# Optimization experiments

Measured on AMD Instinct MI355X. Metric: run time of the kernel, lower is better.

## Reference

```python
import jax, jax.numpy as jnp
import numpy as np

B, L, H = 4, 2048, 1024
NQ, NKV, D = 8, 2, 256
I, V = 3584, 16384
EPS = 1e-6
THETA = 1e7
ROPE_DIM = 64

def rmsnorm(x, w, eps=EPS):
    xf = x.astype(jnp.float32)
    rms = jax.lax.rsqrt(jnp.mean(xf * xf, axis=-1, keepdims=True) + eps)
    return (xf * rms).astype(x.dtype) * w

def apply_rope(x, positions):
    # x: [B, H, L, D]; rotate first ROPE_DIM dims, interleaved pairs
    n_pairs = ROPE_DIM // 2
    inv_freq = THETA ** (-2.0 * jnp.arange(n_pairs, dtype=jnp.float32) / ROPE_DIM)
    freqs = positions.astype(jnp.float32)[:, None] * inv_freq[None, :]  # [L, n_pairs]
    cos = jnp.cos(freqs)[None, None, :, :]
    sin = jnp.sin(freqs)[None, None, :, :]
    b, h, l, d = x.shape
    xr = x[..., :ROPE_DIM].reshape(b, h, l, n_pairs, 2)
    x0, x1 = xr[..., 0], xr[..., 1]
    r0 = x0 * cos - x1 * sin
    r1 = x0 * sin + x1 * cos
    rotated = jnp.stack([r0, r1], axis=-1).reshape(b, h, l, ROPE_DIM)
    return jnp.concatenate([rotated, x[..., ROPE_DIM:]], axis=-1)

def setup_inputs() -> dict:
    key = jax.random.key(0)
    ks = jax.random.split(key, 12)
    s = 0.02
    return {
        "embeddings": jax.random.normal(ks[0], (B, L, H), jnp.float32),
        "hidden_states": jax.random.normal(ks[1], (B, L, H), jnp.float32),
        "pre_emb_w": jnp.ones((H,), jnp.float32),
        "pre_hid_w": jnp.ones((H,), jnp.float32),
        "fc_w": jax.random.normal(ks[2], (H, 2 * H), jnp.float32) * s,
        "in_ln_w": jnp.ones((H,), jnp.float32),
        "q_w": jax.random.normal(ks[3], (2 * NQ * D, H), jnp.float32) * s,
        "k_w": jax.random.normal(ks[4], (NKV * D, H), jnp.float32) * s,
        "v_w": jax.random.normal(ks[5], (NKV * D, H), jnp.float32) * s,
        "o_w": jax.random.normal(ks[6], (H, NQ * D), jnp.float32) * s,
        "qn_w": jnp.ones((D,), jnp.float32),
        "kn_w": jnp.ones((D,), jnp.float32),
        "post_ln_w": jnp.ones((H,), jnp.float32),
        "gate_w": jax.random.normal(ks[7], (I, H), jnp.float32) * s,
        "up_w": jax.random.normal(ks[8], (I, H), jnp.float32) * s,
        "down_w": jax.random.normal(ks[9], (H, I), jnp.float32) * s,
        "norm_w": jnp.ones((H,), jnp.float32),
        "lm_w": jax.random.normal(ks[10], (V, H), jnp.float32) * s,
    }

def _attention(x, q_w, k_w, v_w, o_w, qn_w, kn_w):
    b, l, _ = x.shape
    qg = (x @ q_w.T).reshape(b, l, NQ, 2, D)
    q = qg[:, :, :, 0, :]
    gate = qg[:, :, :, 1, :]
    k = (x @ k_w.T).reshape(b, l, NKV, D)
    v = (x @ v_w.T).reshape(b, l, NKV, D)
    q = rmsnorm(q, qn_w)
    k = rmsnorm(k, kn_w)
    groups = NQ // NKV
    k = jnp.repeat(k, groups, axis=2)  # [B, L, NQ, D]
    v = jnp.repeat(v, groups, axis=2)
    q, k, v = (t.transpose(0, 2, 1, 3) for t in (q, k, v))  # [B, NQ, L, D]
    positions = jnp.arange(l)
    q = apply_rope(q, positions)
    k = apply_rope(k, positions)
    scores = jnp.einsum('bhqd,bhkd->bhqk', q, k) / jnp.sqrt(jnp.float32(D))
    causal = jnp.tril(jnp.ones((l, l), jnp.bool_))
    scores = jnp.where(causal[None, None], scores, jnp.finfo(scores.dtype).min)
    attn = jax.nn.softmax(scores, axis=-1)
    out = jnp.einsum('bhqk,bhkd->bhqd', attn, v)
    out = out.transpose(0, 2, 1, 3).reshape(b, l, NQ * D)
    out = out * jax.nn.sigmoid(gate.reshape(b, l, NQ * D))
    return out @ o_w.T

def reference(embeddings, hidden_states, pre_emb_w, pre_hid_w, fc_w, in_ln_w,
              q_w, k_w, v_w, o_w, qn_w, kn_w, post_ln_w, gate_w, up_w, down_w,
              norm_w, lm_w):
    x = jnp.concatenate([rmsnorm(embeddings, pre_emb_w),
                         rmsnorm(hidden_states, pre_hid_w)], axis=-1)
    x = x @ fc_w.T
    residual = x
    x = rmsnorm(x, in_ln_w)
    x = _attention(x, q_w, k_w, v_w, o_w, qn_w, kn_w)
    x = residual + x
    residual = x
    x = rmsnorm(x, post_ln_w)
    x = (jax.nn.silu(x @ gate_w.T) * (x @ up_w.T)) @ down_w.T
    x = residual + x
    x = rmsnorm(x, norm_w)
    return x @ lm_w.T
```

## Files before the change

### kernel.cpp

```cpp
#include <hip/hip_runtime.h>

typedef __bf16 bf16;
typedef __bf16 bf16x8 __attribute__((ext_vector_type(8)));
typedef __bf16 bf16x4 __attribute__((ext_vector_type(4)));
typedef float f32x4 __attribute__((ext_vector_type(4)));

__device__ inline f32x4 mfma16(bf16x8 a, bf16x8 b, f32x4 c) {
    return __builtin_amdgcn_mfma_f32_16x16x32_bf16(a, b, c, 0, 0, 0);
}

__device__ __forceinline__ void async_cp16(const void* g, void* l) {
    __builtin_amdgcn_global_load_lds(
        (__attribute__((address_space(1))) char*)g,
        (__attribute__((address_space(3))) char*)l,
        16, 0, 0);
}

__global__ __launch_bounds__(256) void w2b_kernel(const float* __restrict__ s,
                                                  bf16* __restrict__ d)
{
    const size_t i = ((size_t)blockIdx.x * 256 + threadIdx.x) * 4;
    const float4 f = *(const float4*)(s + i);
    bf16x4 t;
    t[0] = (bf16)f.x; t[1] = (bf16)f.y; t[2] = (bf16)f.z; t[3] = (bf16)f.w;
    *(bf16x4*)(d + i) = t;
}

__global__ __launch_bounds__(256) void w2b_qkv_kernel(
    const float* __restrict__ qw, const float* __restrict__ kw,
    const float* __restrict__ vw, bf16* __restrict__ dq)
{
    int bid = blockIdx.x;
    const float* s; bf16* d;
    if (bid < 4096)      { s = qw; d = dq; }
    else if (bid < 4608) { s = kw; d = dq + 4194304; bid -= 4096; }
    else                 { s = vw; d = dq + 4718592; bid -= 4608; }
    const size_t i = ((size_t)bid * 256 + threadIdx.x) * 4;
    const float4 f = *(const float4*)(s + i);
    bf16x4 t;
    t[0] = (bf16)f.x; t[1] = (bf16)f.y; t[2] = (bf16)f.z; t[3] = (bf16)f.w;
    *(bf16x4*)(d + i) = t;
}

__global__ __launch_bounds__(256) void w2b_gu_kernel(
    const float* __restrict__ gw, const float* __restrict__ uw, bf16* __restrict__ dg)
{
    int bid = blockIdx.x;
    const float* s; bf16* d;
    if (bid < 3584) { s = gw; d = dg; }
    else            { s = uw; d = dg + 3670016; bid -= 3584; }
    const size_t i = ((size_t)bid * 256 + threadIdx.x) * 4;
    const float4 f = *(const float4*)(s + i);
    bf16x4 t;
    t[0] = (bf16)f.x; t[1] = (bf16)f.y; t[2] = (bf16)f.z; t[3] = (bf16)f.w;
    *(bf16x4*)(d + i) = t;
}

template <int EPI>
__global__ __launch_bounds__(256) void gemm_kernel(
    const bf16* __restrict__ A, const bf16* __restrict__ B,
    const float* __restrict__ res, float* __restrict__ Cout,
    int M, int N, int K)
{
    __shared__ bf16 As[2][128][64];
    __shared__ bf16 Bs[2][128][64];
    const int tid = threadIdx.x;
    const int wave = tid >> 6, lane = tid & 63;
    const int quad = lane >> 4, l16 = lane & 15;
    const int xsw = l16 & 7;

    const int nby = M >> 7, nbx = N >> 7;
    const int nwg = nbx * nby;
    int bid = blockIdx.x;
    {
        const int q = nwg >> 3, r = nwg & 7;
        const int x = bid & 7, loc = bid >> 3;
        bid = (x < r ? x * (q + 1) : r * (q + 1) + (x - r) * q) + loc;
    }
    const int pg = nbx << 3;
    const int g = bid / pg, rem = bid - g * pg;
    const int by = (g << 3) + (rem & 7);
    const int bx = rem >> 3;
    const int row0 = by << 7, col0 = bx << 7;
    const int wrow = ((wave >> 1) << 6), wcol = ((wave & 1) << 6);

    f32x4 acc[4][4] = {};

    const int srow = tid >> 3;
    const int scol = ((tid & 7) ^ (srow & 7)) * 8;
    const bf16* Ag = A + (size_t)(row0 + srow) * K + scol;
    const bf16* Bg = B + (size_t)(col0 + srow) * K + scol;
    const size_t K32 = (size_t)32 * K;

#define STG128(BUF, KB) do { \
    _Pragma("unroll") for (int q = 0; q < 4; ++q) { \
        async_cp16(Ag + q * K32 + (KB), &As[BUF][0][0] + q * 2048 + wave * 512); \
        async_cp16(Bg + q * K32 + (KB), &Bs[BUF][0][0] + q * 2048 + wave * 512); } } while (0)

    const int NT = K >> 6;
    STG128(0, 0);
    __syncthreads();
    for (int t = 0; t < NT; ++t) {
        const int c = t & 1, n = c ^ 1;
        if (t + 1 < NT) STG128(n, (t + 1) * 64);
        bf16x8 af[8], bfr[8];
#pragma unroll
        for (int i = 0; i < 4; ++i) {
            af[i * 2 + 0] = *(const bf16x8*)(&As[c][wrow + i * 16 + l16][(quad ^ xsw) * 8]);
            af[i * 2 + 1] = *(const bf16x8*)(&As[c][wrow + i * 16 + l16][((4 + quad) ^ xsw) * 8]);
        }
#pragma unroll
        for (int j = 0; j < 4; ++j) {
            bfr[j * 2 + 0] = *(const bf16x8*)(&Bs[c][wcol + j * 16 + l16][(quad ^ xsw) * 8]);
            bfr[j * 2 + 1] = *(const bf16x8*)(&Bs[c][wcol + j * 16 + l16][((4 + quad) ^ xsw) * 8]);
        }
#pragma unroll
        for (int i = 0; i < 4; ++i)
#pragma unroll
            for (int j = 0; j < 4; ++j) {
                acc[i][j] = mfma16(af[i * 2 + 0], bfr[j * 2 + 0], acc[i][j]);
                acc[i][j] = mfma16(af[i * 2 + 1], bfr[j * 2 + 1], acc[i][j]);
            }
        __syncthreads();
    }
#undef STG128

#pragma unroll
    for (int i = 0; i < 4; ++i) {
        const int row = row0 + wrow + i * 16 + quad * 4;
#pragma unroll
        for (int j = 0; j < 4; ++j) {
            const int col = col0 + wcol + j * 16 + l16;
#pragma unroll
            for (int r = 0; r < 4; ++r) {
                const size_t idx = (size_t)(row + r) * N + col;
                float v = acc[i][j][r];
                if (EPI == 1) Cout[idx] = v + res[idx];
                else          Cout[idx] = v;
            }
        }
    }
}

template <int EPI>
__global__ __launch_bounds__(512, 2) void gemm256_kernel(
    const bf16* __restrict__ A, const bf16* __restrict__ B,
    const float* __restrict__ res, float* __restrict__ Cout,
    bf16* __restrict__ hout, int M, int N, int K)
{
    __shared__ bf16 As[2][2][128][64];
    __shared__ bf16 Bs[2][2][128][64];
    const int tid = threadIdx.x;
    const int wid = tid >> 6, lane = tid & 63;
    const int quad = lane >> 4, l16 = lane & 15;
    const int wm = wid >> 2, wn = wid & 3;
    const int xsw = l16 & 7;
    const int bofs = (wn & 1) * 64;

    const int nby = M >> 8, nbx = N >> 8;
    const int nwg = nbx * nby;
    int bid = blockIdx.x;
    {
        const int q = nwg >> 3, r = nwg & 7;
        const int x = bid & 7, loc = bid >> 3;
        bid = (x < r ? x * (q + 1) : r * (q + 1) + (x - r) * q) + loc;
    }
    const int pg = nbx << 3;
    const int g = bid / pg, rem = bid - g * pg;
    const int by = (g << 3) + (rem & 7);
    const int bx = rem >> 3;
    const int row0 = by << 8, col0 = bx << 8;

    const int srow = tid >> 3;
    const int scol = ((tid & 7) ^ ((tid >> 3) & 7)) * 8;
    const bf16* Abase = A + (size_t)(row0 + srow) * K + scol;
    const bf16* Bbase = B + (size_t)(col0 + srow) * K + scol;
    const size_t K64 = (size_t)K * 64;
    const size_t K128 = (size_t)K * 128;

    f32x4 acc[8][4] = {};
    bf16x8 af[8], bf0[4], bf1[4];

#define STG_A(BUF, HH, KB) do { \
    const bf16* _g = Abase + (size_t)(HH) * K128 + (KB); \
    bf16* _l = &As[BUF][HH][0][0] + wid * 512; \
    async_cp16(_g, _l); \
    async_cp16(_g + K64, _l + 4096); } while (0)
#define STG_B(BUF, HH, KB) do { \
    const bf16* _g = Bbase + (size_t)(HH) * K128 + (KB); \
    bf16* _l = &Bs[BUF][HH][0][0] + wid * 512; \
    async_cp16(_g, _l); \
    async_cp16(_g + K64, _l + 4096); } while (0)

#define RD_A(BUF, RH) do { \
    const bf16 (*Ah_)[64] = As[BUF][wm]; \
    _Pragma("unroll") for (int f = 0; f < 4; ++f) { \
        af[f*2+0] = *(const bf16x8*)(&Ah_[(RH)*64 + f*16 + l16][(quad ^ xsw) * 8]); \
        af[f*2+1] = *(const bf16x8*)(&Ah_[(RH)*64 + f*16 + l16][((4 + quad) ^ xsw) * 8]); } } while (0)

#define RD_B(BUF, CH, BF) do { \
    const bf16 (*Bh_)[64] = Bs[BUF][wn >> 1]; \
    _Pragma("unroll") for (int f = 0; f < 2; ++f) { \
        BF[f*2+0] = *(const bf16x8*)(&Bh_[bofs + (CH)*32 + f*16 + l16][(quad ^ xsw) * 8]); \
        BF[f*2+1] = *(const bf16x8*)(&Bh_[bofs + (CH)*32 + f*16 + l16][((4 + quad) ^ xsw) * 8]); } } while (0)

#define MFMA_Q(RH, CH, BF) do { \
    _Pragma("unroll") for (int f = 0; f < 4; ++f) \
    _Pragma("unroll") for (int f2 = 0; f2 < 2; ++f2) { \
        acc[(RH)*4+f][(CH)*2+f2] = mfma16(af[f*2+0], BF[f2*2+0], acc[(RH)*4+f][(CH)*2+f2]); \
        acc[(RH)*4+f][(CH)*2+f2] = mfma16(af[f*2+1], BF[f2*2+1], acc[(RH)*4+f][(CH)*2+f2]); } } while (0)

    const int NT = K >> 6;
    STG_A(0, 0, 0); STG_A(0, 1, 0); STG_B(0, 0, 0); STG_B(0, 1, 0);
    if (NT > 1) {
        STG_A(1, 0, 64); STG_A(1, 1, 64); STG_B(1, 0, 64); STG_B(1, 1, 64);
        asm volatile("s_waitcnt vmcnt(8)" ::: "memory");
    } else {
        asm volatile("s_waitcnt vmcnt(0)" ::: "memory");
    }
    __builtin_amdgcn_sched_barrier(0);
    __builtin_amdgcn_s_barrier();
    RD_A(0, 0); RD_B(0, 0, bf0); RD_B(0, 1, bf1);
    __builtin_amdgcn_sched_barrier(0);

    for (int t = 0; t < NT; ++t) {
        const int c = t & 1, n = c ^ 1;
        const int kb1 = (t + 1) << 6, kb2 = (t + 2) << 6;
        if (t >= 1 && t + 1 < NT) { STG_A(n, 0, kb1); STG_A(n, 1, kb1); }
        asm volatile("s_waitcnt lgkmcnt(4)" ::: "memory");
        __builtin_amdgcn_sched_barrier(0);
        __builtin_amdgcn_s_setprio(1);
        MFMA_Q(0, 0, bf0);
        __builtin_amdgcn_s_setprio(0);
        asm volatile("s_waitcnt lgkmcnt(0)" ::: "memory");
        __builtin_amdgcn_sched_barrier(0);
        __builtin_amdgcn_s_setprio(1);
        MFMA_Q(0, 1, bf1);
        __builtin_amdgcn_s_setprio(0);
        RD_A(c, 1);
        __builtin_amdgcn_sched_barrier(0);
        __builtin_amdgcn_s_barrier();
        if (t + 2 < NT) { STG_B(c, 0, kb2); STG_B(c, 1, kb2); }
        asm volatile("s_waitcnt lgkmcnt(0)" ::: "memory");
        __builtin_amdgcn_sched_barrier(0);
        __builtin_amdgcn_s_setprio(1);
        MFMA_Q(1, 0, bf0);
        MFMA_Q(1, 1, bf1);
        __builtin_amdgcn_s_setprio(0);
        if (t + 1 < NT) {
            if (t + 2 < NT) { asm volatile("s_waitcnt vmcnt(4)" ::: "memory"); }
            else            { asm volatile("s_waitcnt vmcnt(0)" ::: "memory"); }
            __builtin_amdgcn_sched_barrier(0);
            RD_A(n, 0); RD_B(n, 0, bf0); RD_B(n, 1, bf1);
            __builtin_amdgcn_sched_barrier(0);
        }
        __builtin_amdgcn_s_barrier();
    }
#undef STG_A
#undef STG_B
#undef RD_A
#undef RD_B
#undef MFMA_Q

#pragma unroll
    for (int fr = 0; fr < 8; ++fr) {
        const int row = row0 + wm * 128 + fr * 16 + quad * 4;
#pragma unroll
        for (int fc = 0; fc < 4; ++fc) {
            const int col = col0 + wn * 64 + fc * 16 + l16;
#pragma unroll
            for (int r = 0; r < 4; ++r) {
                const size_t idx = (size_t)(row + r) * N + col;
                float v = acc[fr][fc][r];
                if (EPI == 1) {
                    Cout[idx] = v + res[idx];
                } else if (EPI == 2) {
                    const float gg = res[idx];
                    hout[idx] = (bf16)(gg * (1.f / (1.f + __expf(-gg))) * v);
                } else {
                    Cout[idx] = v;
                }
            }
        }
    }
}

__global__ __launch_bounds__(256) void prenorm_kernel(
    const float* __restrict__ emb, const float* __restrict__ hid,
    const float* __restrict__ we, const float* __restrict__ wh,
    bf16* __restrict__ xcat)
{
    const int rr = blockIdx.x * 4 + (threadIdx.x >> 6);
    const int lane = threadIdx.x & 63;
    const int half = rr & 1, row = rr >> 1;
    const float* x = (half ? hid : emb) + (size_t)row * 1024;
    const float* w = half ? wh : we;
    float4 v[4]; float ss = 0.f;
#pragma unroll
    for (int j = 0; j < 4; ++j) {
        v[j] = *(const float4*)(x + (size_t)(lane + 64 * j) * 4);
        ss += v[j].x * v[j].x + v[j].y * v[j].y + v[j].z * v[j].z + v[j].w * v[j].w;
    }
#pragma unroll
    for (int m = 32; m; m >>= 1) ss += __shfl_xor(ss, m, 64);
    const float rms = rsqrtf(ss * (1.f / 1024.f) + 1e-6f);
    bf16* o = xcat + (size_t)row * 2048 + half * 1024;
#pragma unroll
    for (int j = 0; j < 4; ++j) {
        const int d = (lane + 64 * j) * 4;
        float4 wv = *(const float4*)(w + d);
        bf16x4 t;
        t[0] = (bf16)(v[j].x * rms * wv.x);
        t[1] = (bf16)(v[j].y * rms * wv.y);
        t[2] = (bf16)(v[j].z * rms * wv.z);
        t[3] = (bf16)(v[j].w * rms * wv.w);
        *(bf16x4*)(o + d) = t;
    }
}

__global__ __launch_bounds__(256) void rmsnorm_kernel(
    const float* __restrict__ xin, const float* __restrict__ w, bf16* __restrict__ out)
{
    const int row = blockIdx.x * 4 + (threadIdx.x >> 6);
    const int lane = threadIdx.x & 63;
    const float* x = xin + (size_t)row * 1024;
    float4 v[4]; float ss = 0.f;
#pragma unroll
    for (int j = 0; j < 4; ++j) {
        v[j] = *(const float4*)(x + (size_t)(lane + 64 * j) * 4);
        ss += v[j].x * v[j].x + v[j].y * v[j].y + v[j].z * v[j].z + v[j].w * v[j].w;
    }
#pragma unroll
    for (int m = 32; m; m >>= 1) ss += __shfl_xor(ss, m, 64);
    const float rms = rsqrtf(ss * (1.f / 1024.f) + 1e-6f);
    bf16* o = out + (size_t)row * 1024;
#pragma unroll
    for (int j = 0; j < 4; ++j) {
        const int d = (lane + 64 * j) * 4;
        float4 wv = *(const float4*)(w + d);
        bf16x4 t;
        t[0] = (bf16)(v[j].x * rms * wv.x);
        t[1] = (bf16)(v[j].y * rms * wv.y);
        t[2] = (bf16)(v[j].z * rms * wv.z);
        t[3] = (bf16)(v[j].w * rms * wv.w);
        *(bf16x4*)(o + d) = t;
    }
}

__global__ __launch_bounds__(256) void qprep_kernel(
    const float* __restrict__ qg, const float* __restrict__ qn_w, bf16* __restrict__ qa)
{
    const int row = blockIdx.x * 4 + (threadIdx.x >> 6);
    const int lane = threadIdx.x & 63;
    const int h = row & 7, bl = row >> 3;
    const int l = bl & 2047, b = bl >> 11;
    const float* x = qg + (size_t)row * 512;
    float4 v = *(const float4*)(x + lane * 4);
    float ss = v.x * v.x + v.y * v.y + v.z * v.z + v.w * v.w;
#pragma unroll
    for (int m = 32; m; m >>= 1) ss += __shfl_xor(ss, m, 64);
    const float rms = rsqrtf(ss * (1.f / 256.f) + 1e-6f);
    const float4 wv = *(const float4*)(qn_w + lane * 4);
    float y0 = v.x * rms * wv.x, y1 = v.y * rms * wv.y;
    float y2 = v.z * rms * wv.z, y3 = v.w * rms * wv.w;
    if (lane < 16) {
        const float inv0 = powf(1e7f, -(float)(4 * lane) * (1.f / 64.f));
        const float inv1 = powf(1e7f, -(float)(4 * lane + 2) * (1.f / 64.f));
        const float a0 = (float)l * inv0, a1 = (float)l * inv1;
        const float c0 = cosf(a0), s0 = sinf(a0), c1 = cosf(a1), s1 = sinf(a1);
        const float r0 = y0 * c0 - y1 * s0, r1 = y0 * s0 + y1 * c0;
        const float r2 = y2 * c1 - y3 * s1, r3 = y2 * s1 + y3 * c1;
        y0 = r0; y1 = r1; y2 = r2; y3 = r3;
    }
    bf16* o = qa + ((size_t)((b * 8 + h) * 2048 + l)) * 256 + lane * 4;
    bf16x4 t;
    t[0] = (bf16)(y0 * 0.0625f); t[1] = (bf16)(y1 * 0.0625f);
    t[2] = (bf16)(y2 * 0.0625f); t[3] = (bf16)(y3 * 0.0625f);
    *(bf16x4*)o = t;
}

__global__ __launch_bounds__(256) void kprep_kernel(
    const float* __restrict__ kvf, const float* __restrict__ kn_w, bf16* __restrict__ ka)
{
    const int row = blockIdx.x * 4 + (threadIdx.x >> 6);
    const int lane = threadIdx.x & 63;
    const int kv = row & 1, bl = row >> 1;
    const int l = bl & 2047, b = bl >> 11;
    const float* x = kvf + (size_t)bl * 1024 + kv * 256;
    float4 v = *(const float4*)(x + lane * 4);
    float ss = v.x * v.x + v.y * v.y + v.z * v.z + v.w * v.w;
#pragma unroll
    for (int m = 32; m; m >>= 1) ss += __shfl_xor(ss, m, 64);
    const float rms = rsqrtf(ss * (1.f / 256.f) + 1e-6f);
    const float4 wv = *(const float4*)(kn_w + lane * 4);
    float y0 = v.x * rms * wv.x, y1 = v.y * rms * wv.y;
    float y2 = v.z * rms * wv.z, y3 = v.w * rms * wv.w;
    if (lane < 16) {
        const float inv0 = powf(1e7f, -(float)(4 * lane) * (1.f / 64.f));
        const float inv1 = powf(1e7f, -(float)(4 * lane + 2) * (1.f / 64.f));
        const float a0 = (float)l * inv0, a1 = (float)l * inv1;
        const float c0 = cosf(a0), s0 = sinf(a0), c1 = cosf(a1), s1 = sinf(a1);
        const float r0 = y0 * c0 - y1 * s0, r1 = y0 * s0 + y1 * c0;
        const float r2 = y2 * c1 - y3 * s1, r3 = y2 * s1 + y3 * c1;
        y0 = r0; y1 = r1; y2 = r2; y3 = r3;
    }
    bf16* o = ka + ((size_t)((b * 2 + kv) * 2048 + l)) * 256 + lane * 4;
    bf16x4 t;
    t[0] = (bf16)y0; t[1] = (bf16)y1; t[2] = (bf16)y2; t[3] = (bf16)y3;
    *(bf16x4*)o = t;
}

__global__ __launch_bounds__(256) void vprep_kernel(const float* __restrict__ kvf,
                                                    bf16* __restrict__ vt)
{
    __shared__ float t[64][65];
    const int l0 = blockIdx.x << 6;
    const int d0 = blockIdx.y << 6;
    const int b = blockIdx.z >> 1, kv = blockIdx.z & 1;
    const int tx = threadIdx.x & 63, ty = threadIdx.x >> 6;
    const float* src = kvf + (size_t)b * 2048 * 1024 + 512 + kv * 256;
#pragma unroll
    for (int j = 0; j < 16; ++j) {
        const int l = ty + j * 4;
        t[l][tx] = src[(size_t)(l0 + l) * 1024 + d0 + tx];
    }
    __syncthreads();
    bf16* dst = vt + (size_t)(b * 2 + kv) * 256 * 2048;
#pragma unroll
    for (int j = 0; j < 16; ++j) {
        const int d = ty + j * 4;
        dst[(size_t)(d0 + d) * 2048 + l0 + tx] = (bf16)t[tx][d];
    }
}

__global__ __launch_bounds__(256) void attn_kernel(
    const bf16* __restrict__ qa, const bf16* __restrict__ ka,
    const bf16* __restrict__ vt, const float* __restrict__ qg,
    bf16* __restrict__ ag)
{
    __shared__ bf16 Ks[32 * 256];
    __shared__ bf16 Vt[256 * 32];
    __shared__ bf16 Pw[4 * 16 * 32];
    const int tid = threadIdx.x;
    const int wave = tid >> 6, lane = tid & 63;
    const int quad = lane >> 4, l16 = lane & 15;
    const int bid = blockIdx.x;
    const int j = bid & 15, h = (bid >> 4) & 7, b = bid >> 7;
    const int kvh = h >> 2;
    const bf16* qptr = qa + ((size_t)(b * 8 + h)) * 2048 * 256;
    const bf16* kptr = ka + ((size_t)(b * 2 + kvh)) * 2048 * 256;
    const bf16* vptr = vt + ((size_t)(b * 2 + kvh)) * 256 * 2048;

    for (int s = 0; s < 2; ++s) {
        const int qt = s ? (31 - j) : j;
        const int qbase = qt * 64 + wave * 16;

        bf16x8 qf[8];
#pragma unroll
        for (int db = 0; db < 8; ++db)
            qf[db] = *(const bf16x8*)(qptr + (size_t)(qbase + l16) * 256 + db * 32 + quad * 8);

        f32x4 o_acc[16] = {};
        float m_i[4], l_i[4];
#pragma unroll
        for (int r = 0; r < 4; ++r) { m_i[r] = -1e30f; l_i[r] = 0.f; }

        const int ntiles = qt * 2 + 2;
        for (int kt = 0; kt < ntiles; ++kt) {
            const int kvs = kt * 32;
#pragma unroll
            for (int c = 0; c < 4; ++c) {
                const int idx = tid + c * 256;
                const int kr = idx >> 5, kc32 = idx & 31;
                *(bf16x8*)(&Ks[kr * 256 + (kc32 ^ (kr & 7)) * 8]) =
                    *(const bf16x8*)(kptr + (size_t)(kvs + kr) * 256 + kc32 * 8);
                const int vd = idx >> 2, vc = (idx & 3) * 8;
                *(bf16x8*)(&Vt[vd * 32 + vc]) = *(const bf16x8*)(vptr + (size_t)vd * 2048 + kvs + vc);
            }
            __syncthreads();

            f32x4 s0 = {}, s1 = {};
#pragma unroll
            for (int db = 0; db < 8; ++db) {
                const int ch = (db * 4 + quad) ^ (l16 & 7);
                bf16x8 k0 = *(const bf16x8*)(&Ks[l16 * 256 + ch * 8]);
                bf16x8 k1 = *(const bf16x8*)(&Ks[(16 + l16) * 256 + ch * 8]);
                s0 = mfma16(qf[db], k0, s0);
                s1 = mfma16(qf[db], k1, s1);
            }

            float alpha[4], p0v[4], p1v[4];
#pragma unroll
            for (int r = 0; r < 4; ++r) {
                const int qrow = qbase + quad * 4 + r;
                float a0 = (kvs + l16 > qrow) ? -1e30f : s0[r];
                float a1 = (kvs + 16 + l16 > qrow) ? -1e30f : s1[r];
                float mx = fmaxf(a0, a1);
#pragma unroll
                for (int m = 8; m; m >>= 1) mx = fmaxf(mx, __shfl_xor(mx, m, 64));
                const float mnew = fmaxf(m_i[r], mx);
                const float a = __expf(m_i[r] - mnew);
                const float p0 = __expf(a0 - mnew);
                const float p1 = __expf(a1 - mnew);
                float ps = p0 + p1;
#pragma unroll
                for (int m = 8; m; m >>= 1) ps += __shfl_xor(ps, m, 64);
                l_i[r] = l_i[r] * a + ps;
                m_i[r] = mnew;
                alpha[r] = a; p0v[r] = p0; p1v[r] = p1;
            }
#pragma unroll
            for (int t = 0; t < 16; ++t) {
                f32x4 o = o_acc[t];
                o[0] *= alpha[0]; o[1] *= alpha[1]; o[2] *= alpha[2]; o[3] *= alpha[3];
                o_acc[t] = o;
            }
            bf16* pw = &Pw[wave * 16 * 32];
#pragma unroll
            for (int r = 0; r < 4; ++r) {
                pw[(quad * 4 + r) * 32 + l16]      = (bf16)p0v[r];
                pw[(quad * 4 + r) * 32 + 16 + l16] = (bf16)p1v[r];
            }
            __syncthreads();
            const bf16x8 pa = *(const bf16x8*)(&pw[l16 * 32 + quad * 8]);
#pragma unroll
            for (int t = 0; t < 16; ++t) {
                bf16x8 vfr = *(const bf16x8*)(&Vt[(t * 16 + l16) * 32 + quad * 8]);
                o_acc[t] = mfma16(pa, vfr, o_acc[t]);
            }
            __syncthreads();
        }

#pragma unroll
        for (int r = 0; r < 4; ++r) {
            const float inv = 1.f / l_i[r];
            const int row = qbase + quad * 4 + r;
            const float* gr = qg + ((size_t)((b * 2048 + row) * 8 + h)) * 512 + 256;
            bf16* ar = ag + ((size_t)(b * 2048 + row)) * 2048 + h * 256;
#pragma unroll
            for (int t = 0; t < 16; ++t) {
                const int d = t * 16 + l16;
                const float o = o_acc[t][r] * inv;
                const float gg = gr[d];
                ar[d] = (bf16)(o * (1.f / (1.f + __expf(-gg))));
            }
        }
    }
}

extern "C" void kernel_launch(void* const* d_in, const int* in_sizes, int n_in,
                              void* d_out, int out_size, void* d_ws, size_t ws_size,
                              hipStream_t stream)
{
    const float* emb       = (const float*)d_in[0];
    const float* hid       = (const float*)d_in[1];
    const float* pre_emb_w = (const float*)d_in[2];
    const float* pre_hid_w = (const float*)d_in[3];
    const float* fc_w      = (const float*)d_in[4];
    const float* in_ln_w   = (const float*)d_in[5];
    const float* q_w       = (const float*)d_in[6];
    const float* k_w       = (const float*)d_in[7];
    const float* v_w       = (const float*)d_in[8];
    const float* o_w       = (const float*)d_in[9];
    const float* qn_w      = (const float*)d_in[10];
    const float* kn_w      = (const float*)d_in[11];
    const float* post_ln_w = (const float*)d_in[12];
    const float* gate_w    = (const float*)d_in[13];
    const float* up_w      = (const float*)d_in[14];
    const float* down_w    = (const float*)d_in[15];
    const float* norm_w    = (const float*)d_in[16];
    const float* lm_w      = (const float*)d_in[17];
    float* out = (float*)d_out;
    char* ws = (char*)d_ws;

    float* xres = (float*)(ws + 0);
    bf16*  xln  = (bf16*)(ws + 33554432);
    char*  C    = ws + 50331648;
    char*  D    = ws + 184549376;
    char*  E    = ws + 318767104;
    float* qg   = (float*)C;
    float* gf   = (float*)C;
    bf16*  xcat = (bf16*)D;
    float* kvf  = (float*)(D + 33554432);
    bf16*  ag   = (bf16*)(D + 67108864);
    bf16*  qa   = (bf16*)E;
    bf16*  ka   = (bf16*)(E + 33554432);
    bf16*  va   = (bf16*)(E + 41943040);
    bf16*  hb   = (bf16*)E;
    bf16*  wbC  = (bf16*)C;
    bf16*  wbD  = (bf16*)D;
    bf16*  wkv  = (bf16*)D + 4194304;
    bf16*  wbDt = (bf16*)(D + 117440512);

    prenorm_kernel<<<4096, 256, 0, stream>>>(emb, hid, pre_emb_w, pre_hid_w, xcat);

    w2b_kernel<<<2048, 256, 0, stream>>>(fc_w, wbC);
    gemm_kernel<0><<<512, 256, 0, stream>>>(xcat, wbC, nullptr, xres, 8192, 1024, 2048);
    rmsnorm_kernel<<<2048, 256, 0, stream>>>(xres, in_ln_w, xln);

    w2b_qkv_kernel<<<5120, 256, 0, stream>>>(q_w, k_w, v_w, wbD);
    gemm256_kernel<0><<<512, 512, 0, stream>>>(xln, wbD, nullptr, qg, nullptr, 8192, 4096, 1024);
    gemm_kernel<0><<<512, 256, 0, stream>>>(xln, wkv, nullptr, kvf, 8192, 1024, 1024);

    qprep_kernel<<<16384, 256, 0, stream>>>(qg, qn_w, qa);
    kprep_kernel<<<4096, 256, 0, stream>>>(kvf, kn_w, ka);
    vprep_kernel<<<dim3(32, 4, 8), 256, 0, stream>>>(kvf, va);
    attn_kernel<<<512, 256, 0, stream>>>(qa, ka, va, qg, ag);

    w2b_kernel<<<2048, 256, 0, stream>>>(o_w, wbC);
    gemm_kernel<1><<<512, 256, 0, stream>>>(ag, wbC, xres, xres, 8192, 1024, 2048);
    rmsnorm_kernel<<<2048, 256, 0, stream>>>(xres, post_ln_w, xln);

    w2b_gu_kernel<<<7168, 256, 0, stream>>>(gate_w, up_w, wbDt);
    gemm256_kernel<0><<<448, 512, 0, stream>>>(xln, wbDt, nullptr, gf, nullptr, 8192, 3584, 1024);
    gemm256_kernel<2><<<448, 512, 0, stream>>>(xln, wbDt + 3670016, gf, nullptr, hb, 8192, 3584, 1024);

    w2b_kernel<<<3584, 256, 0, stream>>>(down_w, wbC);
    gemm_kernel<1><<<512, 256, 0, stream>>>(hb, wbC, xres, xres, 8192, 1024, 3584);
    rmsnorm_kernel<<<2048, 256, 0, stream>>>(xres, norm_w, xln);

    w2b_kernel<<<16384, 256, 0, stream>>>(lm_w, wbC);
    gemm256_kernel<0><<<2048, 512, 0, stream>>>(xln, wbC, nullptr, out, nullptr, 8192, 16384, 1024);
}
```

Before: 1.710 ms.

## Double-buffer K/V tiles in attention via async global-to-LDS loads

The attention kernel now keeps two LDS buffers for K and V tiles. It prefetches the next tile with global_load_lds while the current one is being computed, and swaps explicit waitcnt/barrier sequences in for the __syncthreads calls. The weight-conversion kernel becomes grid-stride with a fixed grid of 2048 blocks, which cuts block count for the large lm_head and down weights. The aim is to hide K/V load latency behind MFMA work. In exchange the kernel uses twice the LDS, which may lower occupancy, and the Pw write/read now relies on an intra-wave lgkmcnt wait rather than a block barrier.

```diff
diff --git a/kernel.cpp b/kernel.cpp
--- a/kernel.cpp
+++ b/kernel.cpp
@@ -17,13 +17,15 @@
 }
 
 __global__ __launch_bounds__(256) void w2b_kernel(const float* __restrict__ s,
-                                                  bf16* __restrict__ d)
-{
-    const size_t i = ((size_t)blockIdx.x * 256 + threadIdx.x) * 4;
-    const float4 f = *(const float4*)(s + i);
-    bf16x4 t;
-    t[0] = (bf16)f.x; t[1] = (bf16)f.y; t[2] = (bf16)f.z; t[3] = (bf16)f.w;
-    *(bf16x4*)(d + i) = t;
+                                                  bf16* __restrict__ d, int nvec4)
+{
+    for (size_t i = (size_t)blockIdx.x * 256 + threadIdx.x; i < (size_t)nvec4;
+         i += (size_t)2048 * 256) {
+        const float4 f = *(const float4*)(s + i * 4);
+        bf16x4 t;
+        t[0] = (bf16)f.x; t[1] = (bf16)f.y; t[2] = (bf16)f.z; t[3] = (bf16)f.w;
+        *(bf16x4*)(d + i * 4) = t;
+    }
 }
 
 __global__ __launch_bounds__(256) void w2b_qkv_kernel(
@@ -438,8 +440,8 @@
     const bf16* __restrict__ vt, const float* __restrict__ qg,
     bf16* __restrict__ ag)
 {
-    __shared__ bf16 Ks[32 * 256];
-    __shared__ bf16 Vt[256 * 32];
+    __shared__ bf16 Ks[2][32 * 256];
+    __shared__ bf16 Vt[2][256 * 32];
     __shared__ bf16 Pw[4 * 16 * 32];
     const int tid = threadIdx.x;
     const int wave = tid >> 6, lane = tid & 63;
@@ -451,6 +453,17 @@
     const bf16* kptr = ka + ((size_t)(b * 2 + kvh)) * 2048 * 256;
     const bf16* vptr = vt + ((size_t)(b * 2 + kvh)) * 256 * 2048;
 
+#define STAGE_KV(BUF, KVS) do { \
+    _Pragma("unroll") for (int c = 0; c < 4; ++c) { \
+        const int idx = c * 256 + tid; \
+        const int kr = idx >> 5; \
+        const int kcs = ((idx & 31) ^ (kr & 7)) * 8; \
+        async_cp16(kptr + (size_t)((KVS) + kr) * 256 + kcs, \
+                   &Ks[BUF][0] + c * 2048 + wave * 512); \
+        const int vd = idx >> 2, vc = (idx & 3) * 8; \
+        async_cp16(vptr + (size_t)vd * 2048 + (KVS) + vc, \
+                   &Vt[BUF][0] + c * 2048 + wave * 512); } } while (0)
+
     for (int s = 0; s < 2; ++s) {
         const int qt = s ? (31 - j) : j;
         const int qbase = qt * 64 + wave * 16;
@@ -466,25 +479,22 @@
         for (int r = 0; r < 4; ++r) { m_i[r] = -1e30f; l_i[r] = 0.f; }
 
         const int ntiles = qt * 2 + 2;
+        STAGE_KV(0, 0);
+        asm volatile("s_waitcnt vmcnt(0)" ::: "memory");
+        __builtin_amdgcn_s_barrier();
+        __builtin_amdgcn_sched_barrier(0);
+
         for (int kt = 0; kt < ntiles; ++kt) {
+            const int cb = kt & 1, nb = cb ^ 1;
             const int kvs = kt * 32;
-#pragma unroll
-            for (int c = 0; c < 4; ++c) {
-                const int idx = tid + c * 256;
-                const int kr = idx >> 5, kc32 = idx & 31;
-                *(bf16x8*)(&Ks[kr * 256 + (kc32 ^ (kr & 7)) * 8]) =
-                    *(const bf16x8*)(kptr + (size_t)(kvs + kr) * 256 + kc32 * 8);
-                const int vd = idx >> 2, vc = (idx & 3) * 8;
-                *(bf16x8*)(&Vt[vd * 32 + vc]) = *(const bf16x8*)(vptr + (size_t)vd * 2048 + kvs + vc);
-            }
-            __syncthreads();
+            if (kt + 1 < ntiles) STAGE_KV(nb, kvs + 32);
 
             f32x4 s0 = {}, s1 = {};
 #pragma unroll
             for (int db = 0; db < 8; ++db) {
                 const int ch = (db * 4 + quad) ^ (l16 & 7);
-                bf16x8 k0 = *(const bf16x8*)(&Ks[l16 * 256 + ch * 8]);
-                bf16x8 k1 = *(const bf16x8*)(&Ks[(16 + l16) * 256 + ch * 8]);
+                bf16x8 k0 = *(const bf16x8*)(&Ks[cb][l16 * 256 + ch * 8]);
+                bf16x8 k1 = *(const bf16x8*)(&Ks[cb][(16 + l16) * 256 + ch * 8]);
                 s0 = mfma16(qf[db], k0, s0);
                 s1 = mfma16(qf[db], k1, s1);
             }
@@ -521,14 +531,17 @@
                 pw[(quad * 4 + r) * 32 + l16]      = (bf16)p0v[r];
                 pw[(quad * 4 + r) * 32 + 16 + l16] = (bf16)p1v[r];
             }
-            __syncthreads();
+            asm volatile("s_waitcnt lgkmcnt(0)" ::: "memory");
+            __builtin_amdgcn_sched_barrier(0);
             const bf16x8 pa = *(const bf16x8*)(&pw[l16 * 32 + quad * 8]);
 #pragma unroll
             for (int t = 0; t < 16; ++t) {
-                bf16x8 vfr = *(const bf16x8*)(&Vt[(t * 16 + l16) * 32 + quad * 8]);
+                bf16x8 vfr = *(const bf16x8*)(&Vt[cb][(t * 16 + l16) * 32 + quad * 8]);
                 o_acc[t] = mfma16(pa, vfr, o_acc[t]);
             }
-            __syncthreads();
+            asm volatile("s_waitcnt vmcnt(0)" ::: "memory");
+            __builtin_amdgcn_s_barrier();
+            __builtin_amdgcn_sched_barrier(0);
         }
 
 #pragma unroll
@@ -546,6 +559,7 @@
             }
         }
     }
+#undef STAGE_KV
 }
 
 extern "C" void kernel_launch(void* const* d_in, const int* in_sizes, int n_in,
@@ -594,7 +608,7 @@
 
     prenorm_kernel<<<4096, 256, 0, stream>>>(emb, hid, pre_emb_w, pre_hid_w, xcat);
 
-    w2b_kernel<<<2048, 256, 0, stream>>>(fc_w, wbC);
+    w2b_kernel<<<2048, 256, 0, stream>>>(fc_w, wbC, 524288);
     gemm_kernel<0><<<512, 256, 0, stream>>>(xcat, wbC, nullptr, xres, 8192, 1024, 2048);
     rmsnorm_kernel<<<2048, 256, 0, stream>>>(xres, in_ln_w, xln);
 
@@ -607,7 +621,7 @@
     vprep_kernel<<<dim3(32, 4, 8), 256, 0, stream>>>(kvf, va);
     attn_kernel<<<512, 256, 0, stream>>>(qa, ka, va, qg, ag);
 
-    w2b_kernel<<<2048, 256, 0, stream>>>(o_w, wbC);
+    w2b_kernel<<<2048, 256, 0, stream>>>(o_w, wbC, 524288);
     gemm_kernel<1><<<512, 256, 0, stream>>>(ag, wbC, xres, xres, 8192, 1024, 2048);
     rmsnorm_kernel<<<2048, 256, 0, stream>>>(xres, post_ln_w, xln);
 
@@ -615,10 +629,10 @@
     gemm256_kernel<0><<<448, 512, 0, stream>>>(xln, wbDt, nullptr, gf, nullptr, 8192, 3584, 1024);
     gemm256_kernel<2><<<448, 512, 0, stream>>>(xln, wbDt + 3670016, gf, nullptr, hb, 8192, 3584, 1024);
 
-    w2b_kernel<<<3584, 256, 0, stream>>>(down_w, wbC);
+    w2b_kernel<<<2048, 256, 0, stream>>>(down_w, wbC, 917504);
     gemm_kernel<1><<<512, 256, 0, stream>>>(hb, wbC, xres, xres, 8192, 1024, 3584);
     rmsnorm_kernel<<<2048, 256, 0, stream>>>(xres, norm_w, xln);
 
-    w2b_kernel<<<16384, 256, 0, stream>>>(lm_w, wbC);
+    w2b_kernel<<<2048, 256, 0, stream>>>(lm_w, wbC, 4194304);
     gemm256_kernel<0><<<2048, 512, 0, stream>>>(xln, wbC, nullptr, out, nullptr, 8192, 16384, 1024);
 }
```

Result: no change. 1.725 ms (+0.9%).
